# Kernel tuning notes

Measured on AMD Instinct MI355X. Metric: run time of the kernel, lower is better.

The kernel has to match this reference:

```python
import jax, jax.numpy as jnp
import numpy as np

S_SCALE = 64.0   # arcface scale
MARGIN = 0.5     # arcface additive angular margin
EMB = 512
NUM_CLASSES = 100000
BATCH = 512


def setup_inputs() -> dict:
    key = jax.random.key(0)
    k1, k2, k3, k4 = jax.random.split(key, 4)
    # xavier_uniform for [num_classes, emb]
    limit = float(np.sqrt(6.0 / (NUM_CLASSES + EMB)))
    weight = jax.random.uniform(k1, (NUM_CLASSES, EMB), jnp.float32, -limit, limit)
    fc_weight = jax.random.uniform(k2, (NUM_CLASSES, EMB), jnp.float32, -limit, limit)
    local_embeddings = jax.random.normal(k3, (BATCH, EMB), jnp.float32)
    local_labels = jax.random.randint(k4, (BATCH,), 0, NUM_CLASSES, jnp.int64)
    return {
        "local_embeddings": local_embeddings,
        "weight": weight,
        "fc_weight": fc_weight,
        "local_labels": local_labels,
        "epoch": 40,
    }


def _l2norm(x, eps=1e-12):
    return x / jnp.maximum(jnp.linalg.norm(x, axis=-1, keepdims=True), eps)


def _arcface(logits, labels):
    # insightface ArcFace: replace target cosine with cos(theta + m), then scale by s
    rows = jnp.arange(logits.shape[0])
    target = logits[rows, labels]
    sin = jnp.sqrt(jnp.maximum(1.0 - target * target, 0.0))
    cos_m, sin_m = jnp.cos(MARGIN), jnp.sin(MARGIN)
    with_margin = target * cos_m - sin * sin_m            # cos(theta + m)
    # safeguard: only apply when theta + m <= pi  (target > cos(pi - m))
    threshold = jnp.cos(jnp.pi - MARGIN)
    mm = jnp.sin(jnp.pi - MARGIN) * MARGIN
    new_target = jnp.where(target > threshold, with_margin, target - mm)
    logits = logits.at[rows, labels].set(new_target)
    return logits * S_SCALE


def _ce(logits, labels):
    rows = jnp.arange(logits.shape[0])
    logp = jax.nn.log_softmax(logits, axis=-1)
    return -jnp.mean(logp[rows, labels])


def reference(local_embeddings, weight, fc_weight, local_labels, epoch):
    labels = local_labels.astype(jnp.int32)
    # margin branch: normalize both sides, cosine logits, arcface margin, CE
    norm_emb = _l2norm(local_embeddings)
    norm_w = _l2norm(weight)
    logits = norm_emb @ norm_w.T                   # [B, num_classes]
    logits = _arcface(logits, labels)
    margin_loss = _ce(logits, labels)
    # plain CE branch on raw linear
    ce_logits = local_embeddings @ fc_weight.T     # [B, num_classes]
    ce_loss = _ce(ce_logits, labels)
    if epoch <= 30:
        return ce_loss + 0.0 * margin_loss
    else:
        return 0.0 * ce_loss + margin_loss
```

## Files before the change

kernel.cpp:

```cpp
#include <hip/hip_runtime.h>

typedef float floatx4 __attribute__((ext_vector_type(4)));
typedef int   intx4   __attribute__((ext_vector_type(4)));
typedef int   intx8   __attribute__((ext_vector_type(8)));

#define NC      100000
#define NCP     100096
#define EMBD    512
#define BATCH   512
#define NCH     782

#define COS_M   0.8775825618903728f
#define SIN_M   0.479425538604203f
#define THRESH  (-0.8775825618903728f)
#define MM_C    0.2397127693021015f

#define GLOAD16(g, l) __builtin_amdgcn_global_load_lds( \
    (const __attribute__((address_space(1))) void*)(g), \
    (__attribute__((address_space(3))) void*)(l), 16, 0, 0)

__device__ __forceinline__ uint2 pack8_fp8(float4 a, float4 b) {
  int lo = 0, hi = 0;
  lo = __builtin_amdgcn_cvt_pk_fp8_f32(a.x, a.y, lo, false);
  lo = __builtin_amdgcn_cvt_pk_fp8_f32(a.z, a.w, lo, true);
  hi = __builtin_amdgcn_cvt_pk_fp8_f32(b.x, b.y, hi, false);
  hi = __builtin_amdgcn_cvt_pk_fp8_f32(b.z, b.w, hi, true);
  return make_uint2((unsigned)lo, (unsigned)hi);
}

__global__ __launch_bounds__(256) void prep_small_k(
    const float* __restrict__ emb, const float* __restrict__ weight,
    const float* __restrict__ fcw, const int* __restrict__ labels,
    const int* __restrict__ epoch, unsigned char* __restrict__ Aq,
    float* __restrict__ tsc, int* __restrict__ lab32,
    float* __restrict__ out) {
  const bool mm = (*epoch > 30);
  const int tid = threadIdx.x;
  const int pred = (labels[2 * tid + 1] != 0) ? 1 : 0;
  const bool is64 = (__syncthreads_or(pred) == 0);

  const int w = tid >> 6, lane = tid & 63;
  const int row = blockIdx.x * 4 + w;
  const int lab = is64 ? labels[2 * row] : labels[row];
  const float* W = mm ? weight : fcw;

  const float* er = emb + (size_t)row * EMBD + lane * 8;
  const float* wr = W + (size_t)lab * EMBD + lane * 8;
  float4 e0 = *(const float4*)er,  e1 = *(const float4*)(er + 4);
  float4 w0 = *(const float4*)wr,  w1 = *(const float4*)(wr + 4);
  float dot = e0.x*w0.x + e0.y*w0.y + e0.z*w0.z + e0.w*w0.w
            + e1.x*w1.x + e1.y*w1.y + e1.z*w1.z + e1.w*w1.w;
  float ssa = e0.x*e0.x + e0.y*e0.y + e0.z*e0.z + e0.w*e0.w
            + e1.x*e1.x + e1.y*e1.y + e1.z*e1.z + e1.w*e1.w;
  float ssw = w0.x*w0.x + w0.y*w0.y + w0.z*w0.z + w0.w*w0.w
            + w1.x*w1.x + w1.y*w1.y + w1.z*w1.z + w1.w*w1.w;
  #pragma unroll
  for (int off = 32; off; off >>= 1) {
    dot += __shfl_xor(dot, off, 64);
    ssa += __shfl_xor(ssa, off, 64);
    ssw += __shfl_xor(ssw, off, 64);
  }
  const float inva = mm ? (1.0f / fmaxf(sqrtf(ssa), 1e-12f)) : 1.0f;
  float4 q0 = make_float4(e0.x*inva, e0.y*inva, e0.z*inva, e0.w*inva);
  float4 q1 = make_float4(e1.x*inva, e1.y*inva, e1.z*inva, e1.w*inva);
  *(uint2*)(Aq + (size_t)row * EMBD + lane * 8) = pack8_fp8(q0, q1);

  if (lane == 0) {
    lab32[row] = lab;
    float tv;
    if (mm) {
      float cosv = dot / (fmaxf(sqrtf(ssa), 1e-12f) * fmaxf(sqrtf(ssw), 1e-12f));
      float sinv = sqrtf(fmaxf(1.0f - cosv * cosv, 0.0f));
      float wmarg = cosv * COS_M - sinv * SIN_M;
      float nt = (cosv > THRESH) ? wmarg : (cosv - MM_C);
      tv = 64.0f * nt;
    } else {
      tv = dot;
    }
    tsc[row] = tv;
  }
  if (blockIdx.x == 0 && tid == 0) out[0] = 0.0f;
}

__global__ __launch_bounds__(256) void prep_w_k(
    const float* __restrict__ weight, const float* __restrict__ fcw,
    const int* __restrict__ epoch, unsigned char* __restrict__ Wq) {
  const bool mm = (*epoch > 30);
  const float* W = mm ? weight : fcw;
  const int w = threadIdx.x >> 6, lane = threadIdx.x & 63;
  const int row = blockIdx.x * 4 + w;
  unsigned char* dst = Wq + (size_t)row * EMBD + lane * 8;
  if (row >= NC) {
    *(uint2*)dst = make_uint2(0u, 0u);
    return;
  }
  const float* src = W + (size_t)row * EMBD + lane * 8;
  float4 a = *(const float4*)src;
  float4 b = *(const float4*)(src + 4);
  float ss = a.x*a.x + a.y*a.y + a.z*a.z + a.w*a.w
           + b.x*b.x + b.y*b.y + b.z*b.z + b.w*b.w;
  #pragma unroll
  for (int off = 32; off; off >>= 1) ss += __shfl_xor(ss, off, 64);
  const float inv = mm ? (1.0f / fmaxf(sqrtf(ss), 1e-12f)) : 1.0f;
  float4 qa = make_float4(a.x*inv, a.y*inv, a.z*inv, a.w*inv);
  float4 qb = make_float4(b.x*inv, b.y*inv, b.z*inv, b.w*inv);
  *(uint2*)dst = pack8_fp8(qa, qb);
}

__global__ __launch_bounds__(256, 2) void gemm_fused_k(
    const unsigned char* __restrict__ Aq, const unsigned char* __restrict__ Wq,
    const float* __restrict__ tsc, const int* __restrict__ lab32,
    const int* __restrict__ epoch, float2* __restrict__ partials) {
  const int t = blockIdx.x & 31, gblk = blockIdx.x >> 5;
  const int bn = gblk * 8 + (t & 7);
  const int bm = t >> 3;
  if (bn >= NCH) return;

  const bool mm = (*epoch > 30);
  const float scale = mm ? 64.0f : 1.0f;

  __shared__ unsigned char As[128 * 128];
  __shared__ unsigned char Bs[128 * 128];
  __shared__ float tscS[128];
  __shared__ int   labS[128];

  const int tid  = threadIdx.x;
  const int lane = tid & 63;
  const int w    = tid >> 6;
  const int m0   = bm * 128;
  const int n0   = bn * 128;

  if (tid < 128) { tscS[tid] = tsc[m0 + tid]; labS[tid] = lab32[m0 + tid]; }

  floatx4 acc[2][8];
  #pragma unroll
  for (int i = 0; i < 2; i++)
    #pragma unroll
    for (int j = 0; j < 8; j++) acc[i][j] = (floatx4){0.f, 0.f, 0.f, 0.f};

  const int rseg = lane >> 3;
  const int swz  = ((lane & 7) ^ rseg) * 16;
  const unsigned char* gA[4];
  const unsigned char* gB[4];
  #pragma unroll
  for (int s = 0; s < 4; s++) {
    gA[s] = Aq + (size_t)(m0 + w * 32 + s * 8 + rseg) * EMBD + swz;
    gB[s] = Wq + (size_t)(n0 + w * 32 + s * 8 + rseg) * EMBD + swz;
  }

  const int rsel = lane & 15;
  const int g2   = (lane >> 4) * 2;
  const int c0   = (g2 ^ (rsel & 7)) * 16;
  const int c1   = ((g2 + 1) ^ (rsel & 7)) * 16;

  for (int kt = 0; kt < 4; ++kt) {
    #pragma unroll
    for (int s = 0; s < 4; s++) {
      GLOAD16(gA[s] + kt * 128, &As[(w * 32 + s * 8) * 128]);
      GLOAD16(gB[s] + kt * 128, &Bs[(w * 32 + s * 8) * 128]);
    }
    __syncthreads();

    intx8 af[2], bv[8];
    #pragma unroll
    for (int mi = 0; mi < 2; mi++) {
      const int base = (w * 32 + mi * 16 + rsel) * 128;
      intx4 lo = *(const intx4*)&As[base + c0];
      intx4 hi = *(const intx4*)&As[base + c1];
      af[mi] = __builtin_shufflevector(lo, hi, 0, 1, 2, 3, 4, 5, 6, 7);
    }
    #pragma unroll
    for (int ni = 0; ni < 8; ni++) {
      const int base = (ni * 16 + rsel) * 128;
      intx4 lo = *(const intx4*)&Bs[base + c0];
      intx4 hi = *(const intx4*)&Bs[base + c1];
      bv[ni] = __builtin_shufflevector(lo, hi, 0, 1, 2, 3, 4, 5, 6, 7);
    }
    #pragma unroll
    for (int mi = 0; mi < 2; mi++)
      #pragma unroll
      for (int ni = 0; ni < 8; ni++)
        acc[mi][ni] = __builtin_amdgcn_mfma_scale_f32_16x16x128_f8f6f4(
            af[mi], bv[ni], acc[mi][ni], 0, 0,
            0, 0x7f7f7f7f, 0, 0x7f7f7f7f);
    __syncthreads();
  }

  const int colq = lane & 15;
  #pragma unroll
  for (int mi = 0; mi < 2; mi++) {
    #pragma unroll
    for (int r = 0; r < 4; r++) {
      const int rl = w * 32 + mi * 16 + (lane >> 4) * 4 + r;
      const int lab = labS[rl];
      const float tv = tscS[rl];
      float v[8];
      #pragma unroll
      for (int ni = 0; ni < 8; ni++) {
        const int cg = n0 + ni * 16 + colq;
        float x = acc[mi][ni][r] * scale;
        if (cg >= NC) x = -1e30f;
        else if (cg == lab) x = tv;
        v[ni] = x;
      }
      float mx = v[0];
      #pragma unroll
      for (int ni = 1; ni < 8; ni++) mx = fmaxf(mx, v[ni]);
      #pragma unroll
      for (int off = 1; off < 16; off <<= 1) mx = fmaxf(mx, __shfl_xor(mx, off, 64));
      float s = 0.0f;
      #pragma unroll
      for (int ni = 0; ni < 8; ni++) s += __expf(v[ni] - mx);
      #pragma unroll
      for (int off = 1; off < 16; off <<= 1) s += __shfl_xor(s, off, 64);
      if (colq == 0)
        partials[(size_t)(m0 + rl) * NCH + bn] = make_float2(mx, s);
    }
  }
}

__global__ __launch_bounds__(256) void rowmerge_k(
    const float2* __restrict__ partials, const float* __restrict__ tsc,
    float* __restrict__ out) {
  const int row = blockIdx.x;
  const int tid = threadIdx.x;
  float M = -1e30f, S = 0.0f;
  for (int j = tid; j < NCH; j += 256) {
    const float2 p = partials[(size_t)row * NCH + j];
    if (p.x > M) { S = S * __expf(M - p.x) + p.y; M = p.x; }
    else         { S += p.y * __expf(p.x - M); }
  }
  __shared__ float sm[256], sv[256];
  sm[tid] = M; sv[tid] = S;
  __syncthreads();
  for (int st = 128; st > 0; st >>= 1) {
    if (tid < st) {
      const float m2 = sm[tid + st], s2 = sv[tid + st];
      const float m1 = sm[tid],      s1 = sv[tid];
      const float Mn = fmaxf(m1, m2);
      sv[tid] = s1 * __expf(m1 - Mn) + s2 * __expf(m2 - Mn);
      sm[tid] = Mn;
    }
    __syncthreads();
  }
  if (tid == 0) {
    const float loss = (sm[0] + __logf(sv[0])) - tsc[row];
    atomicAdd(out, loss * (1.0f / 512.0f));
  }
}

extern "C" void kernel_launch(void* const* d_in, const int* in_sizes, int n_in,
                              void* d_out, int out_size, void* d_ws, size_t ws_size,
                              hipStream_t stream) {
  const float* emb    = (const float*)d_in[0];
  const float* weight = (const float*)d_in[1];
  const float* fcw    = (const float*)d_in[2];
  const int*   labels = (const int*)d_in[3];
  const int*   epoch  = (const int*)d_in[4];
  float* out = (float*)d_out;

  char* ws = (char*)d_ws;
  size_t off = 0;
  unsigned char* Aq = (unsigned char*)(ws + off); off += (size_t)BATCH * EMBD;
  unsigned char* Wq = (unsigned char*)(ws + off); off += (size_t)NCP * EMBD;
  float* tsc       = (float*)(ws + off); off += BATCH * 4;
  int* lab32       = (int*)(ws + off);   off += BATCH * 4;
  float2* partials = (float2*)(ws + off); off += (size_t)BATCH * NCH * 8;

  prep_small_k<<<BATCH / 4, 256, 0, stream>>>(emb, weight, fcw, labels, epoch,
                                              Aq, tsc, lab32, out);
  prep_w_k<<<NCP / 4, 256, 0, stream>>>(weight, fcw, epoch, Wq);
  gemm_fused_k<<<98 * 32, 256, 0, stream>>>(Aq, Wq, tsc, lab32, epoch, partials);
  rowmerge_k<<<BATCH, 256, 0, stream>>>(partials, tsc, out);
}
```

Before: 473.8 us.

## Fuse weight normalization and FP8 quantization into the GEMM kernel

Removes the separate weight-prep kernel and its FP8 intermediate buffer. Each GEMM block now reads fp32 weight rows itself, normalizes and quantizes them to FP8, and stores them in a swizzled LDS tile, with the N tile shrunk to 64 columns. A fragments are loaded straight from global memory rather than through LDS. The aim is to cut a kernel launch and the round trip of the quantized weights through memory. In exchange, fp32 weights are re-read once per M block (four times), and the partials array and merge work double because the column tiles are narrower.

```diff
diff --git a/kernel.cpp b/kernel.cpp
--- a/kernel.cpp
+++ b/kernel.cpp
@@ -5,19 +5,16 @@
 typedef int   intx8   __attribute__((ext_vector_type(8)));
 
 #define NC      100000
-#define NCP     100096
 #define EMBD    512
 #define BATCH   512
-#define NCH     782
+#define BN      64
+#define NCH     1563
+#define NGB     196
 
 #define COS_M   0.8775825618903728f
 #define SIN_M   0.479425538604203f
 #define THRESH  (-0.8775825618903728f)
 #define MM_C    0.2397127693021015f
-
-#define GLOAD16(g, l) __builtin_amdgcn_global_load_lds( \
-    (const __attribute__((address_space(1))) void*)(g), \
-    (__attribute__((address_space(3))) void*)(l), 16, 0, 0)
 
 __device__ __forceinline__ uint2 pack8_fp8(float4 a, float4 b) {
   int lo = 0, hi = 0;
@@ -82,35 +79,11 @@
   if (blockIdx.x == 0 && tid == 0) out[0] = 0.0f;
 }
 
-__global__ __launch_bounds__(256) void prep_w_k(
-    const float* __restrict__ weight, const float* __restrict__ fcw,
-    const int* __restrict__ epoch, unsigned char* __restrict__ Wq) {
-  const bool mm = (*epoch > 30);
-  const float* W = mm ? weight : fcw;
-  const int w = threadIdx.x >> 6, lane = threadIdx.x & 63;
-  const int row = blockIdx.x * 4 + w;
-  unsigned char* dst = Wq + (size_t)row * EMBD + lane * 8;
-  if (row >= NC) {
-    *(uint2*)dst = make_uint2(0u, 0u);
-    return;
-  }
-  const float* src = W + (size_t)row * EMBD + lane * 8;
-  float4 a = *(const float4*)src;
-  float4 b = *(const float4*)(src + 4);
-  float ss = a.x*a.x + a.y*a.y + a.z*a.z + a.w*a.w
-           + b.x*b.x + b.y*b.y + b.z*b.z + b.w*b.w;
-  #pragma unroll
-  for (int off = 32; off; off >>= 1) ss += __shfl_xor(ss, off, 64);
-  const float inv = mm ? (1.0f / fmaxf(sqrtf(ss), 1e-12f)) : 1.0f;
-  float4 qa = make_float4(a.x*inv, a.y*inv, a.z*inv, a.w*inv);
-  float4 qb = make_float4(b.x*inv, b.y*inv, b.z*inv, b.w*inv);
-  *(uint2*)dst = pack8_fp8(qa, qb);
-}
-
 __global__ __launch_bounds__(256, 2) void gemm_fused_k(
-    const unsigned char* __restrict__ Aq, const unsigned char* __restrict__ Wq,
-    const float* __restrict__ tsc, const int* __restrict__ lab32,
-    const int* __restrict__ epoch, float2* __restrict__ partials) {
+    const unsigned char* __restrict__ Aq, const float* __restrict__ weight,
+    const float* __restrict__ fcw, const float* __restrict__ tsc,
+    const int* __restrict__ lab32, const int* __restrict__ epoch,
+    float2* __restrict__ partials) {
   const int t = blockIdx.x & 31, gblk = blockIdx.x >> 5;
   const int bn = gblk * 8 + (t & 7);
   const int bm = t >> 3;
@@ -118,9 +91,9 @@
 
   const bool mm = (*epoch > 30);
   const float scale = mm ? 64.0f : 1.0f;
-
-  __shared__ unsigned char As[128 * 128];
-  __shared__ unsigned char Bs[128 * 128];
+  const float* __restrict__ Wp = mm ? weight : fcw;
+
+  __shared__ unsigned char Bs[BN * EMBD];
   __shared__ float tscS[128];
   __shared__ int   labS[128];
 
@@ -128,50 +101,60 @@
   const int lane = tid & 63;
   const int w    = tid >> 6;
   const int m0   = bm * 128;
-  const int n0   = bn * 128;
+  const int n0   = bn * BN;
 
   if (tid < 128) { tscS[tid] = tsc[m0 + tid]; labS[tid] = lab32[m0 + tid]; }
 
-  floatx4 acc[2][8];
+  #pragma unroll 4
+  for (int rr = 0; rr < 16; ++rr) {
+    const int r    = w * 16 + rr;
+    const int grow = n0 + r;
+    uint2 pq = make_uint2(0u, 0u);
+    if (grow < NC) {
+      const float* src = Wp + (size_t)grow * EMBD + lane * 8;
+      float4 a = *(const float4*)src;
+      float4 b = *(const float4*)(src + 4);
+      float ss = a.x*a.x + a.y*a.y + a.z*a.z + a.w*a.w
+               + b.x*b.x + b.y*b.y + b.z*b.z + b.w*b.w;
+      #pragma unroll
+      for (int off = 32; off; off >>= 1) ss += __shfl_xor(ss, off, 64);
+      const float inv = mm ? (1.0f / fmaxf(sqrtf(ss), 1e-12f)) : 1.0f;
+      float4 qa = make_float4(a.x*inv, a.y*inv, a.z*inv, a.w*inv);
+      float4 qb = make_float4(b.x*inv, b.y*inv, b.z*inv, b.w*inv);
+      pq = pack8_fp8(qa, qb);
+    }
+    const int addr = r * EMBD + ((lane >> 4) << 7)
+                   + (((((lane >> 1) & 7) ^ (r & 7))) << 4) + ((lane & 1) << 3);
+    *(uint2*)&Bs[addr] = pq;
+  }
+  __syncthreads();
+
+  const int rsel = lane & 15;
+  const int g32  = (lane >> 4) * 32;
+  const int c0   = ((((lane >> 4) * 2)     ^ (rsel & 7)) << 4);
+  const int c1   = (((((lane >> 4) * 2)+1) ^ (rsel & 7)) << 4);
+
+  floatx4 acc[2][4];
   #pragma unroll
   for (int i = 0; i < 2; i++)
     #pragma unroll
-    for (int j = 0; j < 8; j++) acc[i][j] = (floatx4){0.f, 0.f, 0.f, 0.f};
-
-  const int rseg = lane >> 3;
-  const int swz  = ((lane & 7) ^ rseg) * 16;
-  const unsigned char* gA[4];
-  const unsigned char* gB[4];
-  #pragma unroll
-  for (int s = 0; s < 4; s++) {
-    gA[s] = Aq + (size_t)(m0 + w * 32 + s * 8 + rseg) * EMBD + swz;
-    gB[s] = Wq + (size_t)(n0 + w * 32 + s * 8 + rseg) * EMBD + swz;
-  }
-
-  const int rsel = lane & 15;
-  const int g2   = (lane >> 4) * 2;
-  const int c0   = (g2 ^ (rsel & 7)) * 16;
-  const int c1   = ((g2 + 1) ^ (rsel & 7)) * 16;
-
+    for (int j = 0; j < 4; j++) acc[i][j] = (floatx4){0.f, 0.f, 0.f, 0.f};
+
+  #pragma unroll
   for (int kt = 0; kt < 4; ++kt) {
-    #pragma unroll
-    for (int s = 0; s < 4; s++) {
-      GLOAD16(gA[s] + kt * 128, &As[(w * 32 + s * 8) * 128]);
-      GLOAD16(gB[s] + kt * 128, &Bs[(w * 32 + s * 8) * 128]);
-    }
-    __syncthreads();
-
-    intx8 af[2], bv[8];
+    intx8 af[2];
     #pragma unroll
     for (int mi = 0; mi < 2; mi++) {
-      const int base = (w * 32 + mi * 16 + rsel) * 128;
-      intx4 lo = *(const intx4*)&As[base + c0];
-      intx4 hi = *(const intx4*)&As[base + c1];
-      af[mi] = __builtin_shufflevector(lo, hi, 0, 1, 2, 3, 4, 5, 6, 7);
-    }
-    #pragma unroll
-    for (int ni = 0; ni < 8; ni++) {
-      const int base = (ni * 16 + rsel) * 128;
+      const unsigned char* ap =
+          Aq + (size_t)(m0 + w * 32 + mi * 16 + rsel) * EMBD + kt * 128 + g32;
+      intx4 alo = *(const intx4*)ap;
+      intx4 ahi = *(const intx4*)(ap + 16);
+      af[mi] = __builtin_shufflevector(alo, ahi, 0, 1, 2, 3, 4, 5, 6, 7);
+    }
+    intx8 bv[4];
+    #pragma unroll
+    for (int ni = 0; ni < 4; ni++) {
+      const int base = (ni * 16 + rsel) * EMBD + kt * 128;
       intx4 lo = *(const intx4*)&Bs[base + c0];
       intx4 hi = *(const intx4*)&Bs[base + c1];
       bv[ni] = __builtin_shufflevector(lo, hi, 0, 1, 2, 3, 4, 5, 6, 7);
@@ -179,11 +162,10 @@
     #pragma unroll
     for (int mi = 0; mi < 2; mi++)
       #pragma unroll
-      for (int ni = 0; ni < 8; ni++)
+      for (int ni = 0; ni < 4; ni++)
         acc[mi][ni] = __builtin_amdgcn_mfma_scale_f32_16x16x128_f8f6f4(
             af[mi], bv[ni], acc[mi][ni], 0, 0,
             0, 0x7f7f7f7f, 0, 0x7f7f7f7f);
-    __syncthreads();
   }
 
   const int colq = lane & 15;
@@ -194,9 +176,9 @@
       const int rl = w * 32 + mi * 16 + (lane >> 4) * 4 + r;
       const int lab = labS[rl];
       const float tv = tscS[rl];
-      float v[8];
-      #pragma unroll
-      for (int ni = 0; ni < 8; ni++) {
+      float v[4];
+      #pragma unroll
+      for (int ni = 0; ni < 4; ni++) {
         const int cg = n0 + ni * 16 + colq;
         float x = acc[mi][ni][r] * scale;
         if (cg >= NC) x = -1e30f;
@@ -205,12 +187,12 @@
       }
       float mx = v[0];
       #pragma unroll
-      for (int ni = 1; ni < 8; ni++) mx = fmaxf(mx, v[ni]);
+      for (int ni = 1; ni < 4; ni++) mx = fmaxf(mx, v[ni]);
       #pragma unroll
       for (int off = 1; off < 16; off <<= 1) mx = fmaxf(mx, __shfl_xor(mx, off, 64));
       float s = 0.0f;
       #pragma unroll
-      for (int ni = 0; ni < 8; ni++) s += __expf(v[ni] - mx);
+      for (int ni = 0; ni < 4; ni++) s += __expf(v[ni] - mx);
       #pragma unroll
       for (int off = 1; off < 16; off <<= 1) s += __shfl_xor(s, off, 64);
       if (colq == 0)
@@ -262,14 +244,13 @@
   char* ws = (char*)d_ws;
   size_t off = 0;
   unsigned char* Aq = (unsigned char*)(ws + off); off += (size_t)BATCH * EMBD;
-  unsigned char* Wq = (unsigned char*)(ws + off); off += (size_t)NCP * EMBD;
   float* tsc       = (float*)(ws + off); off += BATCH * 4;
   int* lab32       = (int*)(ws + off);   off += BATCH * 4;
   float2* partials = (float2*)(ws + off); off += (size_t)BATCH * NCH * 8;
 
   prep_small_k<<<BATCH / 4, 256, 0, stream>>>(emb, weight, fcw, labels, epoch,
                                               Aq, tsc, lab32, out);
-  prep_w_k<<<NCP / 4, 256, 0, stream>>>(weight, fcw, epoch, Wq);
-  gemm_fused_k<<<98 * 32, 256, 0, stream>>>(Aq, Wq, tsc, lab32, epoch, partials);
+  gemm_fused_k<<<NGB * 32, 256, 0, stream>>>(Aq, weight, fcw, tsc, lab32, epoch,
+                                             partials);
   rowmerge_k<<<BATCH, 256, 0, stream>>>(partials, tsc, out);
 }
```

Measured after the change: 564.5 us. 1.19x slower.
